# Kernel optimization log

Hardware: AMD Instinct MI355X
Metric: run time of the kernel (lower is better)

## Reference

```python
import jax, jax.numpy as jnp
import numpy as np

B, S, H, E, V, T, OOV = 32, 400, 256, 300, 50000, 20, 50


def setup_inputs() -> dict:
    key = jax.random.key(0)
    ks = jax.random.split(key, 24)
    g = lambda k, sh, scale=0.02: jax.random.normal(k, sh, dtype=jnp.float32) * scale
    return {
        "enc_hidden": jax.random.normal(ks[0], (B, S, 2 * H), dtype=jnp.float32),
        "h0": jax.random.normal(ks[1], (B, H), dtype=jnp.float32),
        "c0": jax.random.normal(ks[2], (B, H), dtype=jnp.float32),
        "embedding": g(ks[3], (V, E), 1.0),
        "W_enc": g(ks[4], (2 * H, H)),
        "W_dec": g(ks[5], (H, H)),
        "w_cov": g(ks[6], (H,)),
        "v_attn": g(ks[7], (H,)),
        "W_ih": g(ks[8], (E, 4 * H)),
        "W_hh": g(ks[9], (H, 4 * H)),
        "b_lstm": jnp.zeros((4 * H,), jnp.float32),
        "W_out1": g(ks[10], (3 * H, H)),
        "b_out1": jnp.zeros((H,), jnp.float32),
        "W_out2": g(ks[11], (H, V)),
        "b_out2": jnp.zeros((V,), jnp.float32),
        "w_h": g(ks[12], (2 * H, 1)),
        "w_s": g(ks[13], (H, 1)),
        "w_x": g(ks[14], (E, 1)),
        "b_x": jnp.zeros((1,), jnp.float32),
        "dec_input": jax.random.randint(ks[15], (B, T), 0, V),
        "enc_input_ext": jax.random.randint(ks[16], (B, S), 0, V + OOV),
        "enc_pad_mask": jnp.ones((B, S), dtype=bool),
        "max_oov_len": OOV,
    }


def reference(enc_hidden, h0, c0, embedding, W_enc, W_dec, w_cov, v_attn,
              W_ih, W_hh, b_lstm, W_out1, b_out1, W_out2, b_out2,
              w_h, w_s, w_x, b_x, dec_input, enc_input_ext, enc_pad_mask,
              max_oov_len):
    b, s, two_h = enc_hidden.shape
    enc_feat = enc_hidden @ W_enc  # [B,S,H], precomputed attention keys
    batch_idx = jnp.arange(b)[:, None]
    NEG = jnp.float32(-1e9)

    def step(carry, x_t):
        h, c, cov = carry
        emb = embedding[x_t]  # [B,E]
        # LSTM cell
        gates = emb @ W_ih + h @ W_hh + b_lstm
        i, f, gg, o = jnp.split(gates, 4, axis=-1)
        c = jax.nn.sigmoid(f) * c + jax.nn.sigmoid(i) * jnp.tanh(gg)
        h = jax.nn.sigmoid(o) * jnp.tanh(c)
        # coverage attention over encoder states
        e = jnp.tanh(enc_feat + (h @ W_dec)[:, None, :] + cov[..., None] * w_cov) @ v_attn  # [B,S]
        e = jnp.where(enc_pad_mask, e, NEG)
        attn = jax.nn.softmax(e, axis=-1)
        context = jnp.einsum('bs,bsd->bd', attn, enc_hidden)  # [B,2H]
        cov = cov + attn
        # vocab distribution
        out = jnp.concatenate([h, context], axis=-1) @ W_out1 + b_out1
        vocab_dist = jax.nn.softmax(out @ W_out2 + b_out2, axis=-1)  # [B,V]
        # pointer-generator gate
        p_gen = jax.nn.sigmoid(context @ w_h + h @ w_s + emb @ w_x + b_x)  # [B,1]
        vocab_dist = p_gen * vocab_dist
        weighted_attn = (1.0 - p_gen) * attn
        # extend vocab and scatter-add copy probabilities
        ext = jnp.concatenate(
            [vocab_dist, jnp.zeros((b, max_oov_len), vocab_dist.dtype)], axis=-1)
        final = ext.at[batch_idx, enc_input_ext].add(weighted_attn)
        return (h, c, cov), (final, attn, cov)

    cov0 = jnp.zeros((b, s), jnp.float32)
    _, (finals, attns, covs) = jax.lax.scan(step, (h0, c0, cov0), dec_input.T)
    # stack with time on the last axis, as in the torch module
    return (jnp.moveaxis(finals, 0, -1),
            jnp.moveaxis(attns, 0, -1),
            jnp.moveaxis(covs, 0, -1))
```

## Files before the change

### kernel.cpp

```cpp
#include <hip/hip_runtime.h>
#include <hip/hip_bf16.h>

#define B_    32
#define S_    400
#define H_    256
#define E_    300
#define V_    50000
#define T_    20
#define VE_   50050
#define TB_   640
#define VPAD_ 50048
#define FIN_  32032000
#define NB_   16
#define SC_   25

typedef __attribute__((ext_vector_type(8))) short bf16x8;
typedef __attribute__((ext_vector_type(4))) float f32x4;

__device__ __forceinline__ float sigmoid_f(float x){ return 1.f/(1.f+__expf(-x)); }
__device__ __forceinline__ float tanh_f(float x){ return 1.f - 2.f/(__expf(2.f*x)+1.f); }

__device__ __forceinline__ float bf2f(unsigned short u){
  union { unsigned int i; float f; } x; x.i = ((unsigned int)u) << 16; return x.f;
}
__device__ __forceinline__ unsigned short f2bf(float f){
  union { __hip_bfloat16 h; unsigned short u; } x; x.h = __float2bfloat16(f); return x.u;
}

__device__ __forceinline__ void st_dev(float* p, float v){
  __hip_atomic_store(p, v, __ATOMIC_RELAXED, __HIP_MEMORY_SCOPE_AGENT);
}
__device__ __forceinline__ float ld_dev(const float* p){
  return __hip_atomic_load(p, __ATOMIC_RELAXED, __HIP_MEMORY_SCOPE_AGENT);
}

__device__ __forceinline__ void rowbar(int* cnt, int target){
  __syncthreads();
  if (threadIdx.x == 0){
    asm volatile("s_waitcnt vmcnt(0)" ::: "memory");
    __hip_atomic_fetch_add(cnt, 1, __ATOMIC_RELAXED, __HIP_MEMORY_SCOPE_AGENT);
    while (__hip_atomic_load(cnt, __ATOMIC_RELAXED, __HIP_MEMORY_SCOPE_AGENT) < target){
      __builtin_amdgcn_s_sleep(1);
    }
  }
  __syncthreads();
}


__global__ __launch_bounds__(256) void kc1(const float* __restrict__ in,
                                           __hip_bfloat16* __restrict__ out){
  size_t g = (size_t)blockIdx.x*256 + threadIdx.x;
  float4 f = ((const float4*)in)[g];
  size_t o = g*4;
  out[o+0] = __float2bfloat16(f.x);
  out[o+1] = __float2bfloat16(f.y);
  out[o+2] = __float2bfloat16(f.z);
  out[o+3] = __float2bfloat16(f.w);
}

__global__ __launch_bounds__(256) void kT(const float* __restrict__ in,
                                          __hip_bfloat16* __restrict__ out, int R, int C){
  __shared__ float tile[32][33];
  int tx = threadIdx.x & 31, ty = threadIdx.x >> 5;
  int c = blockIdx.x*32 + tx;
  #pragma unroll
  for (int i = 0; i < 4; ++i){
    int r = blockIdx.y*32 + ty + i*8;
    if (r < R && c < C) tile[ty + i*8][tx] = in[(size_t)r*C + c];
  }
  __syncthreads();
  int r2 = blockIdx.y*32 + tx;
  #pragma unroll
  for (int i = 0; i < 4; ++i){
    int c2 = blockIdx.x*32 + ty + i*8;
    if (r2 < R && c2 < C) out[(size_t)c2*R + r2] = __float2bfloat16(tile[tx][ty + i*8]);
  }
}

__global__ __launch_bounds__(256) void kpair(const float* __restrict__ in,
                                             unsigned short* __restrict__ out, int N){
  int g = blockIdx.x*256 + threadIdx.x;
  int k = g / N, n = g % N;
  out[(size_t)(k >> 1)*(2*N) + n*2 + (k & 1)] = f2bf(in[g]);
}

__global__ __launch_bounds__(256) void k1(const float* __restrict__ emb,
                                          const int* __restrict__ dec,
                                          const float* __restrict__ W_ih,
                                          const float* __restrict__ b_lstm,
                                          float* __restrict__ pre_ih){
  int tid = threadIdx.x;
  int n0 = blockIdx.x*64, m0 = blockIdx.y*64;
  __shared__ float A_s[64][21];
  __shared__ float B_s[20][65];
  __shared__ int gid_s[64];
  if (tid < 64){
    int r = m0 + tid;
    gid_s[tid] = dec[(r & 31)*20 + (r >> 5)];
  }
  float acc[4][4] = {};
  int ty = tid >> 4, tx = tid & 15;
  for (int kc = 0; kc < 15; ++kc){
    __syncthreads();
    for (int e = tid; e < 1280; e += 256){
      int row = e / 20, kk = e % 20;
      A_s[row][kk] = emb[(size_t)gid_s[row]*300 + kc*20 + kk];
    }
    for (int e = tid; e < 1280; e += 256){
      int kk = e >> 6, c = e & 63;
      B_s[kk][c] = W_ih[(size_t)(kc*20 + kk)*1024 + n0 + c];
    }
    __syncthreads();
    #pragma unroll
    for (int kk = 0; kk < 20; ++kk){
      float av[4], bv[4];
      #pragma unroll
      for (int i = 0; i < 4; ++i) av[i] = A_s[ty*4 + i][kk];
      #pragma unroll
      for (int j = 0; j < 4; ++j) bv[j] = B_s[kk][tx*4 + j];
      #pragma unroll
      for (int i = 0; i < 4; ++i)
        #pragma unroll
        for (int j = 0; j < 4; ++j) acc[i][j] += av[i]*bv[j];
    }
  }
  #pragma unroll
  for (int i = 0; i < 4; ++i)
    #pragma unroll
    for (int j = 0; j < 4; ++j){
      int rr = m0 + ty*4 + i, cc = n0 + tx*4 + j;
      pre_ih[(size_t)rr*1024 + cc] = acc[i][j] + b_lstm[cc];
    }
}

__global__ __launch_bounds__(64) void k1b(const float* __restrict__ emb,
                                          const int* __restrict__ dec,
                                          const float* __restrict__ w_x,
                                          const float* __restrict__ b_x,
                                          float* __restrict__ pre_x){
  int r = blockIdx.x, lane = threadIdx.x;
  int gid = dec[(r & 31)*20 + (r >> 5)];
  float p = 0.f;
  for (int k = lane; k < 300; k += 64) p += emb[(size_t)gid*300 + k]*w_x[k];
  #pragma unroll
  for (int off = 32; off > 0; off >>= 1) p += __shfl_xor(p, off);
  if (lane == 0) pre_x[r] = p + b_x[0];
}

__global__ __launch_bounds__(256) void k2(const __hip_bfloat16* __restrict__ Abf,
                                          const __hip_bfloat16* __restrict__ Bt,
                                          __hip_bfloat16* __restrict__ Cbf){
  int tid = threadIdx.x;
  int lane = tid & 63, wave = tid >> 6;
  int wm = wave >> 1, wn = wave & 1;
  int n0 = blockIdx.x*128, m0 = blockIdx.y*128;
  __shared__ __align__(16) unsigned short A_s[128][40];
  __shared__ __align__(16) unsigned short B_s[128][40];
  f32x4 acc[4][4];
  #pragma unroll
  for (int i = 0; i < 4; ++i)
    #pragma unroll
    for (int j = 0; j < 4; ++j) acc[i][j] = (f32x4){0.f,0.f,0.f,0.f};
  int cg = tid & 3;
  for (int kc = 0; kc < 16; ++kc){
    __syncthreads();
    #pragma unroll
    for (int rr = 0; rr < 2; ++rr){
      int row = (tid >> 2) + rr*64;
      *(float4*)&A_s[row][cg*8] = *(const float4*)(Abf + (size_t)(m0+row)*512 + kc*32 + cg*8);
      *(float4*)&B_s[row][cg*8] = *(const float4*)(Bt  + (size_t)(n0+row)*512 + kc*32 + cg*8);
    }
    __syncthreads();
    bf16x8 af[4], bfr[4];
    #pragma unroll
    for (int mt = 0; mt < 4; ++mt)
      af[mt] = *(const bf16x8*)&A_s[wm*64 + mt*16 + (lane & 15)][(lane >> 4)*8];
    #pragma unroll
    for (int nt = 0; nt < 4; ++nt)
      bfr[nt] = *(const bf16x8*)&B_s[wn*64 + nt*16 + (lane & 15)][(lane >> 4)*8];
    #pragma unroll
    for (int mt = 0; mt < 4; ++mt)
      #pragma unroll
      for (int nt = 0; nt < 4; ++nt)
        acc[mt][nt] = __builtin_amdgcn_mfma_f32_16x16x32_bf16(af[mt], bfr[nt], acc[mt][nt], 0, 0, 0);
  }
  int lm = lane & 15, lq = lane >> 4;
  #pragma unroll
  for (int mt = 0; mt < 4; ++mt)
    #pragma unroll
    for (int nt = 0; nt < 4; ++nt){
      int vv = n0 + wn*64 + nt*16 + lm;
      #pragma unroll
      for (int rg = 0; rg < 4; ++rg){
        int r = m0 + wm*64 + mt*16 + lq*4 + rg;
        Cbf[(size_t)r*256 + vv] = __float2bfloat16(acc[mt][nt][rg]);
      }
    }
}

__global__ __launch_bounds__(256) void krec(
    const float* __restrict__ h0, const float* __restrict__ c0,
    const unsigned short* __restrict__ Whh2,
    const unsigned short* __restrict__ Wd2,
    const float* __restrict__ w_cov, const float* __restrict__ v_attn,
    const float* __restrict__ pre_ih, const __hip_bfloat16* __restrict__ enc_feat,
    const float* __restrict__ enc_hidden,
    float* __restrict__ H_all, float* __restrict__ exps_g,
    float* __restrict__ Zatt, float* __restrict__ ctxp,
    float* __restrict__ hdecp, int* bar)
{
  const int bx = blockIdx.x;
  const int b = bx >> 4, jj = bx & 15;
  const int tid = threadIdx.x;
  const int lane = tid & 63, wave = tid >> 6;
  const int s0 = jj*SC_;

  __shared__ __align__(16) unsigned short eh_s[SC_][512];
  __shared__ __align__(16) unsigned short ef_s[SC_][256];
  __shared__ float h_sh[256], hdec_sh[256], vat[256], wcv[256];
  __shared__ float h_loc[16];
  __shared__ float covf[32], ehist[2][32];
  __shared__ float invZ_sh;

  for (int e = tid; e < SC_*128; e += 256){
    int row = e >> 7, c4 = e & 127;
    float4 f = *(const float4*)(enc_hidden + ((size_t)(b*400 + s0 + row))*512 + c4*4);
    unsigned int lo = ((unsigned int)f2bf(f.y) << 16) | f2bf(f.x);
    unsigned int hi = ((unsigned int)f2bf(f.w) << 16) | f2bf(f.z);
    *(unsigned int*)&eh_s[row][c4*4]     = lo;
    *(unsigned int*)&eh_s[row][c4*4 + 2] = hi;
  }
  for (int e = tid; e < SC_*32; e += 256){
    int row = e >> 5, c8 = e & 31;
    *(float4*)&ef_s[row][c8*8] =
      *(const float4*)(enc_feat + ((size_t)(b*400 + s0 + row))*256 + c8*8);
  }
  vat[tid] = v_attn[tid];
  wcv[tid] = w_cov[tid];
  h_sh[tid] = h0[b*256 + tid];
  if (tid < 32) covf[tid] = 0.f;

  const int kq = lane & 3, cl = (lane >> 2) & 3, gt = lane >> 4;
  const int ci = wave*4 + cl;
  const int gcol = gt*256 + jj*16 + ci;
  ushort2 wreg[32];
  #pragma unroll
  for (int pp = 0; pp < 32; ++pp)
    wreg[pp] = *(const ushort2*)(Whh2 + ((size_t)(kq*32 + pp))*2048 + gcol*2);
  ushort2 wdreg[8];
  #pragma unroll
  for (int p = 0; p < 8; ++p)
    wdreg[p] = *(const ushort2*)(Wd2 + ((size_t)(jj*8 + p))*512 + tid*2);
  float c_reg = c0[b*256 + jj*16 + ci];

  __syncthreads();

  int* cnt = bar + b*16;

  #pragma unroll 1
  for (int t = 0; t < T_; ++t){
    const int r = t*32 + b;
    float acc = (kq == 0) ? pre_ih[(size_t)r*1024 + gcol] : 0.f;
    #pragma unroll
    for (int pp = 0; pp < 32; ++pp){
      float2 h2 = *(const float2*)&h_sh[kq*64 + pp*2];
      acc += h2.x*bf2f(wreg[pp].x) + h2.y*bf2f(wreg[pp].y);
    }
    acc += __shfl_xor(acc, 1);
    acc += __shfl_xor(acc, 2);
    {
      int base = lane & 12;
      float gi = __shfl(acc, base);
      float gf = __shfl(acc, base + 16);
      float gG = __shfl(acc, base + 32);
      float go = __shfl(acc, base + 48);
      float cn = sigmoid_f(gf)*c_reg + sigmoid_f(gi)*tanh_f(gG);
      c_reg = cn;
      float hv = sigmoid_f(go)*tanh_f(cn);
      if ((lane & 51) == 0){
        st_dev(&H_all[(size_t)r*256 + jj*16 + ci], hv);
        h_loc[ci] = hv;
      }
    }
    __syncthreads();
    {
      float pd = 0.f;
      #pragma unroll
      for (int p = 0; p < 8; ++p)
        pd += h_loc[p*2]*bf2f(wdreg[p].x) + h_loc[p*2 + 1]*bf2f(wdreg[p].y);
      st_dev(&hdecp[((size_t)r*16 + jj)*256 + tid], pd);
    }
    rowbar(cnt, NB_*(t + 1));
    {
      float hfull = ld_dev(&H_all[(size_t)r*256 + tid]);
      float hd = 0.f;
      #pragma unroll
      for (int j2 = 0; j2 < 16; ++j2)
        hd += ld_dev(&hdecp[((size_t)r*16 + j2)*256 + tid]);
      h_sh[tid] = hfull;
      hdec_sh[tid] = hd;
      if (tid == 0 && t > 0) invZ_sh = 1.f/ld_dev(&Zatt[r - 32]);
    }
    __syncthreads();
    float* ecur = ehist[t & 1];
    const float* eprev = ehist[(t ^ 1) & 1];
    for (int sl = wave; sl < SC_; sl += 4){
      float cw = covf[sl];
      if (t > 0) cw += eprev[sl]*invZ_sh;
      float part = 0.f;
      #pragma unroll
      for (int q = 0; q < 4; ++q){
        int k = lane + q*64;
        float x = bf2f(ef_s[sl][k]) + hdec_sh[k] + cw*wcv[k];
        part += vat[k]*tanh_f(x);
      }
      #pragma unroll
      for (int off = 32; off > 0; off >>= 1) part += __shfl_xor(part, off);
      if (lane == 0){
        covf[sl] = cw;
        float ev = __expf(part);
        ecur[sl] = ev;
        exps_g[(size_t)r*400 + s0 + sl] = ev;
      }
    }
    __syncthreads();
    if (tid == 0){
      float z = 0.f;
      #pragma unroll
      for (int q = 0; q < SC_; ++q) z += ecur[q];
      atomicAdd(&Zatt[r], z);
    }
    #pragma unroll
    for (int hh = 0; hh < 2; ++hh){
      int d = tid + hh*256;
      float a2 = 0.f;
      #pragma unroll
      for (int sl = 0; sl < SC_; ++sl) a2 += ecur[sl]*bf2f(eh_s[sl][d]);
      ctxp[((size_t)r*16 + jj)*512 + d] = a2;
    }
  }
}

__global__ __launch_bounds__(256) void k3a(const float* __restrict__ Zatt,
                                           const float* __restrict__ ctxp,
                                           const float* __restrict__ H_all,
                                           const float* __restrict__ w_h,
                                           const float* __restrict__ w_s,
                                           const float* __restrict__ pre_x,
                                           float* __restrict__ CAT,
                                           float* __restrict__ pgen){
  int r = blockIdx.x, tid = threadIdx.x;
  __shared__ float red[256];
  float invz = 1.f/Zatt[r];
  float hv = H_all[(size_t)r*256 + tid];
  CAT[(size_t)r*768 + tid] = hv;
  float a0 = 0.f, a1 = 0.f;
  const float* p = ctxp + (size_t)r*16*512;
  #pragma unroll
  for (int jj = 0; jj < 16; ++jj){
    a0 += p[jj*512 + tid];
    a1 += p[jj*512 + 256 + tid];
  }
  float cv0 = a0*invz;
  float cv1 = a1*invz;
  CAT[(size_t)r*768 + 256 + tid] = cv0;
  CAT[(size_t)r*768 + 512 + tid] = cv1;
  float pg = hv*w_s[tid] + cv0*w_h[tid] + cv1*w_h[tid + 256];
  red[tid] = pg; __syncthreads();
  for (int st = 128; st > 0; st >>= 1){
    if (tid < st) red[tid] += red[tid + st];
    __syncthreads();
  }
  if (tid == 0) pgen[r] = sigmoid_f(red[0] + pre_x[r]);
}

__global__ __launch_bounds__(256) void k3b(const float* __restrict__ exps_g,
                                           const float* __restrict__ Zatt,
                                           float* __restrict__ attns,
                                           float* __restrict__ covs){
  __shared__ float tA[256*20];
  __shared__ float tC[256*20];
  int tid = threadIdx.x;
  int g0 = blockIdx.x*256;
  int g = g0 + tid;
  int b = g / 400, s = g % 400;
  float cum = 0.f;
  for (int t = 0; t < T_; ++t){
    int r = t*32 + b;
    float a = exps_g[(size_t)r*400 + s] / Zatt[r];
    cum += a;
    tA[tid*20 + t] = a;
    tC[tid*20 + t] = cum;
  }
  __syncthreads();
  size_t base = (size_t)g0*20;
  for (int e = tid; e < 5120; e += 256){
    attns[base + e] = tA[e];
    covs[base + e]  = tC[e];
  }
}

__global__ __launch_bounds__(256) void k4(const float* __restrict__ CAT,
                                          const float* __restrict__ W_out1,
                                          const float* __restrict__ b_out1,
                                          __hip_bfloat16* __restrict__ OUTb){
  int tid = threadIdx.x;
  int n0 = blockIdx.x*64, m0 = blockIdx.y*64;
  __shared__ float A_s[64][17];
  __shared__ float B_s[16][65];
  float acc[4][4] = {};
  int ty = tid >> 4, tx = tid & 15;
  for (int kc = 0; kc < 48; ++kc){
    __syncthreads();
    for (int e = tid; e < 1024; e += 256){
      int row = e >> 4, kk = e & 15;
      A_s[row][kk] = CAT[(size_t)(m0 + row)*768 + kc*16 + kk];
    }
    for (int e = tid; e < 1024; e += 256){
      int kk = e >> 6, c = e & 63;
      B_s[kk][c] = W_out1[(size_t)(kc*16 + kk)*256 + n0 + c];
    }
    __syncthreads();
    #pragma unroll
    for (int kk = 0; kk < 16; ++kk){
      float av[4], bv[4];
      #pragma unroll
      for (int i = 0; i < 4; ++i) av[i] = A_s[ty*4 + i][kk];
      #pragma unroll
      for (int j = 0; j < 4; ++j) bv[j] = B_s[kk][tx*4 + j];
      #pragma unroll
      for (int i = 0; i < 4; ++i)
        #pragma unroll
        for (int j = 0; j < 4; ++j) acc[i][j] += av[i]*bv[j];
    }
  }
  #pragma unroll
  for (int i = 0; i < 4; ++i)
    #pragma unroll
    for (int j = 0; j < 4; ++j){
      int rr = m0 + ty*4 + i, cc = n0 + tx*4 + j;
      OUTb[(size_t)rr*256 + cc] = __float2bfloat16(acc[i][j] + b_out1[cc]);
    }
}

__global__ __launch_bounds__(256) void k5(const __hip_bfloat16* __restrict__ OUTb,
                                          const __hip_bfloat16* __restrict__ W2t,
                                          const float* __restrict__ b_out2,
                                          __hip_bfloat16* __restrict__ temp,
                                          float* __restrict__ Zsum){
  int tid = threadIdx.x;
  int lane = tid & 63, wave = tid >> 6;
  int wm = wave >> 1, wn = wave & 1;
  int n0 = blockIdx.y*128, m0 = blockIdx.x*128;
  __shared__ __align__(16) unsigned short A_s[128][40];
  __shared__ __align__(16) unsigned short B_s[128][40];
  f32x4 acc[4][4];
  #pragma unroll
  for (int i = 0; i < 4; ++i)
    #pragma unroll
    for (int j = 0; j < 4; ++j) acc[i][j] = (f32x4){0.f,0.f,0.f,0.f};
  int cg = tid & 3;
  for (int kc = 0; kc < 8; ++kc){
    __syncthreads();
    #pragma unroll
    for (int rr = 0; rr < 2; ++rr){
      int row = (tid >> 2) + rr*64;
      *(float4*)&A_s[row][cg*8] = *(const float4*)(OUTb + (size_t)(m0 + row)*256 + kc*32 + cg*8);
      int v = n0 + row;
      float4 bv = make_float4(0.f, 0.f, 0.f, 0.f);
      if (v < V_) bv = *(const float4*)(W2t + (size_t)v*256 + kc*32 + cg*8);
      *(float4*)&B_s[row][cg*8] = bv;
    }
    __syncthreads();
    bf16x8 af[4], bfr[4];
    #pragma unroll
    for (int mt = 0; mt < 4; ++mt)
      af[mt] = *(const bf16x8*)&A_s[wm*64 + mt*16 + (lane & 15)][(lane >> 4)*8];
    #pragma unroll
    for (int nt = 0; nt < 4; ++nt)
      bfr[nt] = *(const bf16x8*)&B_s[wn*64 + nt*16 + (lane & 15)][(lane >> 4)*8];
    #pragma unroll
    for (int mt = 0; mt < 4; ++mt)
      #pragma unroll
      for (int nt = 0; nt < 4; ++nt)
        acc[mt][nt] = __builtin_amdgcn_mfma_f32_16x16x32_bf16(af[mt], bfr[nt], acc[mt][nt], 0, 0, 0);
  }
  int lm = lane & 15, lq = lane >> 4;
  float rowsum[4][4];
  #pragma unroll
  for (int mt = 0; mt < 4; ++mt)
    #pragma unroll
    for (int rg = 0; rg < 4; ++rg) rowsum[mt][rg] = 0.f;
  #pragma unroll
  for (int mt = 0; mt < 4; ++mt)
    #pragma unroll
    for (int nt = 0; nt < 4; ++nt){
      int vv = n0 + wn*64 + nt*16 + lm;
      float b2 = (vv < V_) ? b_out2[vv] : 0.f;
      #pragma unroll
      for (int rg = 0; rg < 4; ++rg){
        int r = m0 + wm*64 + mt*16 + lq*4 + rg;
        float e = __expf(acc[mt][nt][rg] + b2);
        temp[(size_t)r*VPAD_ + vv] = __float2bfloat16(e);
        if (vv >= V_) e = 0.f;
        rowsum[mt][rg] += e;
      }
    }
  #pragma unroll
  for (int mt = 0; mt < 4; ++mt)
    #pragma unroll
    for (int rg = 0; rg < 4; ++rg){
      float s = rowsum[mt][rg];
      s += __shfl_xor(s, 1); s += __shfl_xor(s, 2);
      s += __shfl_xor(s, 4); s += __shfl_xor(s, 8);
      if (lm == 0){
        int r = m0 + wm*64 + mt*16 + lq*4 + rg;
        atomicAdd(&Zsum[r], s);
      }
    }
}

__global__ __launch_bounds__(256) void k6(const __hip_bfloat16* __restrict__ temp,
                                          const float* __restrict__ pgen,
                                          const float* __restrict__ Zsum,
                                          float* __restrict__ finals){
  int b = blockIdx.y, cb = blockIdx.x, tid = threadIdx.x;
  int v0 = cb*512;
  __shared__ float tile[20][513];
  __shared__ float ssc[20];
  if (tid < 20){ int r = tid*32 + b; ssc[tid] = pgen[r]/Zsum[r]; }
  __syncthreads();
  for (int e = tid; e < 1280; e += 256){
    int tt = e >> 6, c8 = e & 63;
    int v = v0 + c8*8;
    float sc = ssc[tt];
    const __hip_bfloat16* src = temp + (size_t)(tt*32 + b)*VPAD_ + v;
    if (v + 7 < V_){
      float4 raw = *(const float4*)src;
      const unsigned short* u = (const unsigned short*)&raw;
      #pragma unroll
      for (int j = 0; j < 8; ++j) tile[tt][c8*8 + j] = bf2f(u[j])*sc;
    } else {
      #pragma unroll
      for (int j = 0; j < 8; ++j)
        tile[tt][c8*8 + j] = (v + j < V_) ? __bfloat162float(src[j])*sc : 0.f;
    }
  }
  __syncthreads();
  int wlim = (VE_ - v0)*20; if (wlim > 10240) wlim = 10240;
  float* dst = finals + (size_t)b*1001000 + (size_t)v0*20;
  for (int e = tid; e < wlim; e += 256){
    dst[e] = tile[e % 20][e / 20];
  }
}

__global__ __launch_bounds__(320) void k7(const float* __restrict__ exps_g,
                                          const float* __restrict__ Zatt,
                                          const float* __restrict__ pgen,
                                          const int* __restrict__ ext,
                                          float* __restrict__ finals){
  int tid = threadIdx.x;
  int g = blockIdx.x*16 + tid/20;
  int t = tid % 20;
  int b = g / 400, s = g % 400;
  int r = t*32 + b;
  int idx = ext[g];
  float w = (1.f - pgen[r])*exps_g[(size_t)r*400 + s]/Zatt[r];
  atomicAdd(finals + (size_t)b*1001000 + (size_t)idx*20 + t, w);
}

extern "C" void kernel_launch(void* const* d_in, const int* in_sizes, int n_in,
                              void* d_out, int out_size, void* d_ws, size_t ws_size,
                              hipStream_t stream){
  const float* enc_hidden = (const float*)d_in[0];
  const float* h0         = (const float*)d_in[1];
  const float* c0         = (const float*)d_in[2];
  const float* embedding  = (const float*)d_in[3];
  const float* W_enc      = (const float*)d_in[4];
  const float* W_dec      = (const float*)d_in[5];
  const float* w_cov      = (const float*)d_in[6];
  const float* v_attn     = (const float*)d_in[7];
  const float* W_ih       = (const float*)d_in[8];
  const float* W_hh       = (const float*)d_in[9];
  const float* b_lstm     = (const float*)d_in[10];
  const float* W_out1     = (const float*)d_in[11];
  const float* b_out1     = (const float*)d_in[12];
  const float* W_out2     = (const float*)d_in[13];
  const float* b_out2     = (const float*)d_in[14];
  const float* w_h        = (const float*)d_in[15];
  const float* w_s        = (const float*)d_in[16];
  const float* w_x        = (const float*)d_in[17];
  const float* b_x        = (const float*)d_in[18];
  const int*   dec_input  = (const int*)d_in[19];
  const int*   enc_ext    = (const int*)d_in[20];

  float* out    = (float*)d_out;
  float* finals = out;
  float* attns  = out + FIN_;
  float* covs   = out + FIN_ + 256000;

  char* w = (char*)d_ws;
  auto alloc = [&](size_t n){ char* p = w; w += (n + 255) & ~(size_t)255; return p; };
  int*   bar      = (int*)  alloc(32*64);
  float* Zsum     = (float*)alloc((size_t)TB_*4);
  float* Zatt     = (float*)alloc((size_t)TB_*4);
  float* pre_ih   = (float*)alloc((size_t)TB_*1024*4);
  float* pre_x    = (float*)alloc((size_t)TB_*4);
  unsigned short* Whh2 = (unsigned short*)alloc((size_t)256*1024*2);
  unsigned short* Wd2  = (unsigned short*)alloc((size_t)256*256*2);
  __hip_bfloat16* enc_bf   = (__hip_bfloat16*)alloc((size_t)12800*512*2);
  __hip_bfloat16* WencT    = (__hip_bfloat16*)alloc((size_t)256*512*2);
  __hip_bfloat16* W2t      = (__hip_bfloat16*)alloc((size_t)V_*256*2);
  __hip_bfloat16* enc_feat = (__hip_bfloat16*)alloc((size_t)12800*256*2);
  float* H_all    = (float*)alloc((size_t)TB_*256*4);
  float* exps_g   = (float*)alloc((size_t)TB_*400*4);
  float* CAT      = (float*)alloc((size_t)TB_*768*4);
  float* pgen     = (float*)alloc((size_t)TB_*4);
  __hip_bfloat16* OUTb = (__hip_bfloat16*)alloc((size_t)TB_*256*2);
  __hip_bfloat16* temp = (__hip_bfloat16*)alloc((size_t)TB_*VPAD_*2);
  float* ctxp     = (float*)temp;
  float* hdecp    = (float*)((char*)temp + (size_t)TB_*16*512*4);

  hipMemsetAsync(bar, 0, 32*64, stream);
  hipMemsetAsync(Zsum, 0, (size_t)TB_*4, stream);
  hipMemsetAsync(Zatt, 0, (size_t)TB_*4, stream);

  kc1<<<6400, 256, 0, stream>>>(enc_hidden, enc_bf);
  kT <<<dim3(8, 16), 256, 0, stream>>>(W_enc, WencT, 512, 256);
  kT <<<dim3(1563, 8), 256, 0, stream>>>(W_out2, W2t, 256, V_);
  kpair<<<1024, 256, 0, stream>>>(W_hh, Whh2, 1024);
  kpair<<<256, 256, 0, stream>>>(W_dec, Wd2, 256);
  k1 <<<dim3(16, 10), 256, 0, stream>>>(embedding, dec_input, W_ih, b_lstm, pre_ih);
  k1b<<<640, 64, 0, stream>>>(embedding, dec_input, w_x, b_x, pre_x);
  k2 <<<dim3(2, 100), 256, 0, stream>>>(enc_bf, WencT, enc_feat);
  krec<<<512, 256, 0, stream>>>(h0, c0, Whh2, Wd2, w_cov, v_attn, pre_ih,
                                enc_feat, enc_hidden,
                                H_all, exps_g, Zatt, ctxp, hdecp, bar);
  k3a<<<640, 256, 0, stream>>>(Zatt, ctxp, H_all, w_h, w_s, pre_x, CAT, pgen);
  k3b<<<50, 256, 0, stream>>>(exps_g, Zatt, attns, covs);
  k4 <<<dim3(4, 10), 256, 0, stream>>>(CAT, W_out1, b_out1, OUTb);
  k5 <<<dim3(5, 391), 256, 0, stream>>>(OUTb, W2t, b_out2, temp, Zsum);
  k6 <<<dim3(98, 32), 256, 0, stream>>>(temp, pgen, Zsum, finals);
  k7 <<<800, 320, 0, stream>>>(exps_g, Zatt, pgen, enc_ext, finals);
}
```

Baseline: 904.7 us.

## Fuse prep kernels, convert enc_hidden inside GEMM, remap recurrent blocks, prefetch pre_ih

Drops the separate fp32-to-bf16 conversion of enc_hidden and converts it while loading tiles in the enc_feat GEMM. The two weight-pairing launches become one kernel, and the w_x dot product moves from its own kernel into k3a. The recurrent kernel remaps blocks so each batch row's chunks are spread across the grid, pads the shared h buffer to avoid bank conflicts, and prefetches the next step's pre_ih value. The aim is fewer launches, less intermediate memory traffic and lower latency per recurrent step, at the cost of more conversion work inside the GEMM's load path.

Result: faster. 859.4 us (-5.0%).

```diff
diff --git a/kernel.cpp b/kernel.cpp
--- a/kernel.cpp
+++ b/kernel.cpp
@@ -47,17 +47,6 @@
 }
 
 
-__global__ __launch_bounds__(256) void kc1(const float* __restrict__ in,
-                                           __hip_bfloat16* __restrict__ out){
-  size_t g = (size_t)blockIdx.x*256 + threadIdx.x;
-  float4 f = ((const float4*)in)[g];
-  size_t o = g*4;
-  out[o+0] = __float2bfloat16(f.x);
-  out[o+1] = __float2bfloat16(f.y);
-  out[o+2] = __float2bfloat16(f.z);
-  out[o+3] = __float2bfloat16(f.w);
-}
-
 __global__ __launch_bounds__(256) void kT(const float* __restrict__ in,
                                           __hip_bfloat16* __restrict__ out, int R, int C){
   __shared__ float tile[32][33];
@@ -77,11 +66,19 @@
   }
 }
 
-__global__ __launch_bounds__(256) void kpair(const float* __restrict__ in,
-                                             unsigned short* __restrict__ out, int N){
+__global__ __launch_bounds__(256) void kpair2(const float* __restrict__ Whh,
+                                              const float* __restrict__ Wdec,
+                                              unsigned short* __restrict__ oW,
+                                              unsigned short* __restrict__ oD){
   int g = blockIdx.x*256 + threadIdx.x;
-  int k = g / N, n = g % N;
-  out[(size_t)(k >> 1)*(2*N) + n*2 + (k & 1)] = f2bf(in[g]);
+  if (g < 262144){
+    int k = g >> 10, n = g & 1023;
+    oW[(size_t)(k >> 1)*2048 + n*2 + (k & 1)] = f2bf(Whh[g]);
+  } else {
+    int g2 = g - 262144;
+    int k = g2 >> 8, n = g2 & 255;
+    oD[(size_t)(k >> 1)*512 + n*2 + (k & 1)] = f2bf(Wdec[g2]);
+  }
 }
 
 __global__ __launch_bounds__(256) void k1(const float* __restrict__ emb,
@@ -133,21 +130,7 @@
     }
 }
 
-__global__ __launch_bounds__(64) void k1b(const float* __restrict__ emb,
-                                          const int* __restrict__ dec,
-                                          const float* __restrict__ w_x,
-                                          const float* __restrict__ b_x,
-                                          float* __restrict__ pre_x){
-  int r = blockIdx.x, lane = threadIdx.x;
-  int gid = dec[(r & 31)*20 + (r >> 5)];
-  float p = 0.f;
-  for (int k = lane; k < 300; k += 64) p += emb[(size_t)gid*300 + k]*w_x[k];
-  #pragma unroll
-  for (int off = 32; off > 0; off >>= 1) p += __shfl_xor(p, off);
-  if (lane == 0) pre_x[r] = p + b_x[0];
-}
-
-__global__ __launch_bounds__(256) void k2(const __hip_bfloat16* __restrict__ Abf,
+__global__ __launch_bounds__(256) void k2(const float* __restrict__ EH,
                                           const __hip_bfloat16* __restrict__ Bt,
                                           __hip_bfloat16* __restrict__ Cbf){
   int tid = threadIdx.x;
@@ -167,8 +150,16 @@
     #pragma unroll
     for (int rr = 0; rr < 2; ++rr){
       int row = (tid >> 2) + rr*64;
-      *(float4*)&A_s[row][cg*8] = *(const float4*)(Abf + (size_t)(m0+row)*512 + kc*32 + cg*8);
-      *(float4*)&B_s[row][cg*8] = *(const float4*)(Bt  + (size_t)(n0+row)*512 + kc*32 + cg*8);
+      const float* src = EH + (size_t)(m0+row)*512 + kc*32 + cg*8;
+      float4 f0 = *(const float4*)src;
+      float4 f1 = *(const float4*)(src + 4);
+      unsigned int u0 = ((unsigned int)f2bf(f0.y) << 16) | f2bf(f0.x);
+      unsigned int u1 = ((unsigned int)f2bf(f0.w) << 16) | f2bf(f0.z);
+      unsigned int u2 = ((unsigned int)f2bf(f1.y) << 16) | f2bf(f1.x);
+      unsigned int u3 = ((unsigned int)f2bf(f1.w) << 16) | f2bf(f1.z);
+      unsigned int* dst = (unsigned int*)&A_s[row][cg*8];
+      dst[0] = u0; dst[1] = u1; dst[2] = u2; dst[3] = u3;
+      *(float4*)&B_s[row][cg*8] = *(const float4*)(Bt + (size_t)(n0+row)*512 + kc*32 + cg*8);
     }
     __syncthreads();
     bf16x8 af[4], bfr[4];
@@ -210,14 +201,16 @@
     float* __restrict__ hdecp, int* bar)
 {
   const int bx = blockIdx.x;
-  const int b = bx >> 4, jj = bx & 15;
+  const int b = (bx & 7) + 8*((bx >> 3) & 3);
+  const int jj = bx >> 5;
   const int tid = threadIdx.x;
   const int lane = tid & 63, wave = tid >> 6;
   const int s0 = jj*SC_;
 
   __shared__ __align__(16) unsigned short eh_s[SC_][512];
   __shared__ __align__(16) unsigned short ef_s[SC_][256];
-  __shared__ float h_sh[256], hdec_sh[256], vat[256], wcv[256];
+  __shared__ float h_pad[272];
+  __shared__ float hdec_sh[256], vat[256], wcv[256];
   __shared__ float h_loc[16];
   __shared__ float covf[32], ehist[2][32];
   __shared__ float invZ_sh;
@@ -237,7 +230,7 @@
   }
   vat[tid] = v_attn[tid];
   wcv[tid] = w_cov[tid];
-  h_sh[tid] = h0[b*256 + tid];
+  h_pad[tid + 4*(tid >> 6)] = h0[b*256 + tid];
   if (tid < 32) covf[tid] = 0.f;
 
   const int kq = lane & 3, cl = (lane >> 2) & 3, gt = lane >> 4;
@@ -257,14 +250,21 @@
 
   int* cnt = bar + b*16;
 
+  float pih = (kq == 0) ? pre_ih[(size_t)b*1024 + gcol] : 0.f;
+
   #pragma unroll 1
   for (int t = 0; t < T_; ++t){
     const int r = t*32 + b;
-    float acc = (kq == 0) ? pre_ih[(size_t)r*1024 + gcol] : 0.f;
-    #pragma unroll
-    for (int pp = 0; pp < 32; ++pp){
-      float2 h2 = *(const float2*)&h_sh[kq*64 + pp*2];
-      acc += h2.x*bf2f(wreg[pp].x) + h2.y*bf2f(wreg[pp].y);
+    const int rn = (t < T_-1) ? r + 32 : r;
+    float pih_next = (kq == 0) ? pre_ih[(size_t)rn*1024 + gcol] : 0.f;
+    float acc = pih;
+    {
+      const float* hb = &h_pad[kq*68];
+      #pragma unroll
+      for (int pp = 0; pp < 32; ++pp){
+        float2 h2 = *(const float2*)&hb[pp*2];
+        acc += h2.x*bf2f(wreg[pp].x) + h2.y*bf2f(wreg[pp].y);
+      }
     }
     acc += __shfl_xor(acc, 1);
     acc += __shfl_xor(acc, 2);
@@ -297,7 +297,7 @@
       #pragma unroll
       for (int j2 = 0; j2 < 16; ++j2)
         hd += ld_dev(&hdecp[((size_t)r*16 + j2)*256 + tid]);
-      h_sh[tid] = hfull;
+      h_pad[tid + 4*(tid >> 6)] = hfull;
       hdec_sh[tid] = hd;
       if (tid == 0 && t > 0) invZ_sh = 1.f/ld_dev(&Zatt[r - 32]);
     }
@@ -338,6 +338,7 @@
       for (int sl = 0; sl < SC_; ++sl) a2 += ecur[sl]*bf2f(eh_s[sl][d]);
       ctxp[((size_t)r*16 + jj)*512 + d] = a2;
     }
+    pih = pih_next;
   }
 }
 
@@ -346,7 +347,10 @@
                                            const float* __restrict__ H_all,
                                            const float* __restrict__ w_h,
                                            const float* __restrict__ w_s,
-                                           const float* __restrict__ pre_x,
+                                           const float* __restrict__ emb,
+                                           const int* __restrict__ dec,
+                                           const float* __restrict__ w_x,
+                                           const float* __restrict__ b_x,
                                            float* __restrict__ CAT,
                                            float* __restrict__ pgen){
   int r = blockIdx.x, tid = threadIdx.x;
@@ -365,13 +369,16 @@
   float cv1 = a1*invz;
   CAT[(size_t)r*768 + 256 + tid] = cv0;
   CAT[(size_t)r*768 + 512 + tid] = cv1;
+  int gid = dec[(r & 31)*20 + (r >> 5)];
+  float px = 0.f;
+  for (int k = tid; k < 300; k += 256) px += emb[(size_t)gid*300 + k]*w_x[k];
   float pg = hv*w_s[tid] + cv0*w_h[tid] + cv1*w_h[tid + 256];
-  red[tid] = pg; __syncthreads();
+  red[tid] = pg + px; __syncthreads();
   for (int st = 128; st > 0; st >>= 1){
     if (tid < st) red[tid] += red[tid + st];
     __syncthreads();
   }
-  if (tid == 0) pgen[r] = sigmoid_f(red[0] + pre_x[r]);
+  if (tid == 0) pgen[r] = sigmoid_f(red[0] + b_x[0]);
 }
 
 __global__ __launch_bounds__(256) void k3b(const float* __restrict__ exps_g,
@@ -605,10 +612,8 @@
   float* Zsum     = (float*)alloc((size_t)TB_*4);
   float* Zatt     = (float*)alloc((size_t)TB_*4);
   float* pre_ih   = (float*)alloc((size_t)TB_*1024*4);
-  float* pre_x    = (float*)alloc((size_t)TB_*4);
   unsigned short* Whh2 = (unsigned short*)alloc((size_t)256*1024*2);
   unsigned short* Wd2  = (unsigned short*)alloc((size_t)256*256*2);
-  __hip_bfloat16* enc_bf   = (__hip_bfloat16*)alloc((size_t)12800*512*2);
   __hip_bfloat16* WencT    = (__hip_bfloat16*)alloc((size_t)256*512*2);
   __hip_bfloat16* W2t      = (__hip_bfloat16*)alloc((size_t)V_*256*2);
   __hip_bfloat16* enc_feat = (__hip_bfloat16*)alloc((size_t)12800*256*2);
@@ -625,18 +630,16 @@
   hipMemsetAsync(Zsum, 0, (size_t)TB_*4, stream);
   hipMemsetAsync(Zatt, 0, (size_t)TB_*4, stream);
 
-  kc1<<<6400, 256, 0, stream>>>(enc_hidden, enc_bf);
   kT <<<dim3(8, 16), 256, 0, stream>>>(W_enc, WencT, 512, 256);
   kT <<<dim3(1563, 8), 256, 0, stream>>>(W_out2, W2t, 256, V_);
-  kpair<<<1024, 256, 0, stream>>>(W_hh, Whh2, 1024);
-  kpair<<<256, 256, 0, stream>>>(W_dec, Wd2, 256);
+  kpair2<<<1280, 256, 0, stream>>>(W_hh, W_dec, Whh2, Wd2);
   k1 <<<dim3(16, 10), 256, 0, stream>>>(embedding, dec_input, W_ih, b_lstm, pre_ih);
-  k1b<<<640, 64, 0, stream>>>(embedding, dec_input, w_x, b_x, pre_x);
-  k2 <<<dim3(2, 100), 256, 0, stream>>>(enc_bf, WencT, enc_feat);
+  k2 <<<dim3(2, 100), 256, 0, stream>>>(enc_hidden, WencT, enc_feat);
   krec<<<512, 256, 0, stream>>>(h0, c0, Whh2, Wd2, w_cov, v_attn, pre_ih,
                                 enc_feat, enc_hidden,
                                 H_all, exps_g, Zatt, ctxp, hdecp, bar);
-  k3a<<<640, 256, 0, stream>>>(Zatt, ctxp, H_all, w_h, w_s, pre_x, CAT, pgen);
+  k3a<<<640, 256, 0, stream>>>(Zatt, ctxp, H_all, w_h, w_s,
+                               embedding, dec_input, w_x, b_x, CAT, pgen);
   k3b<<<50, 256, 0, stream>>>(exps_g, Zatt, attns, covs);
   k4 <<<dim3(4, 10), 256, 0, stream>>>(CAT, W_out1, b_out1, OUTb);
   k5 <<<dim3(5, 391), 256, 0, stream>>>(OUTb, W2t, b_out2, temp, Zsum);
```
